# Kernel optimization log

Measured on AMD Instinct MI355X. Metric: run time of the kernel, lower is better.

Reference implementation:

```python
import jax, jax.numpy as jnp
import numpy as np

D_MODEL = 1024
D_HIDDEN = 4096
NUM_EXPERTS = 8
TOP_K = 2


def setup_inputs() -> dict:
    key = jax.random.key(0)
    ks = jax.random.split(key, 7)
    scale_in = 1.0 / np.sqrt(D_MODEL)
    scale_hid = 1.0 / np.sqrt(D_HIDDEN)
    x = jax.random.normal(ks[0], (4, 2048, D_MODEL), dtype=jnp.float32)
    Wr = jax.random.uniform(ks[1], (D_MODEL, NUM_EXPERTS), jnp.float32, -scale_in, scale_in)
    br = jax.random.uniform(ks[2], (NUM_EXPERTS,), jnp.float32, -scale_in, scale_in)
    W1 = jax.random.uniform(ks[3], (NUM_EXPERTS, D_MODEL, D_HIDDEN), jnp.float32, -scale_in, scale_in)
    b1 = jax.random.uniform(ks[4], (NUM_EXPERTS, D_HIDDEN), jnp.float32, -scale_in, scale_in)
    W2 = jax.random.uniform(ks[5], (NUM_EXPERTS, D_HIDDEN, D_MODEL), jnp.float32, -scale_hid, scale_hid)
    b2 = jax.random.uniform(ks[6], (NUM_EXPERTS, D_MODEL), jnp.float32, -scale_hid, scale_hid)
    return {"x": x, "Wr": Wr, "br": br, "W1": W1, "b1": b1, "W2": W2, "b2": b2}


def reference(x, Wr, br, W1, b1, W2, b2):
    B, S, D = x.shape
    E = Wr.shape[1]
    flat = x.reshape(-1, D)                      # [T, D]
    T = flat.shape[0]
    logits = flat @ Wr + br                      # [T, E]
    probs = jax.nn.softmax(logits, axis=-1)
    topk_p, topk_i = jax.lax.top_k(probs, TOP_K)  # [T, K]
    topk_p = topk_p / jnp.sum(topk_p, axis=-1, keepdims=True)
    # combine[t, e] = sum_k topk_p[t, k] * (topk_i[t, k] == e)
    combine = jnp.zeros((T, E), flat.dtype).at[jnp.arange(T)[:, None], topk_i].add(topk_p)
    out = jnp.zeros_like(flat)
    for e in range(E):  # fixed small expert loop; each iter is a dense GEMM pair
        h = jax.nn.relu(flat @ W1[e] + b1[e])    # [T, d_hidden]
        y = h @ W2[e] + b2[e]                    # [T, D]
        out = out + y * combine[:, e:e + 1]
    return out.reshape(B, S, D)
```

## Files before the change

kernel.cpp:

```cpp
#include <hip/hip_runtime.h>
#include <stdint.h>

#define D_MODEL  1024
#define D_HIDDEN 4096
#define NE       8
#define T_TOK    8192
#define BM       128
#define BN       128
#define MAXT     136
#define ROWS_CAP 17408

typedef __attribute__((ext_vector_type(8))) short short8;
typedef __attribute__((ext_vector_type(4))) float f32x4;

__device__ inline uint16_t f2bf(float f) {
  uint32_t u = __float_as_uint(f);
  uint32_t r = (u + 0x7fffu + ((u >> 16) & 1u)) >> 16;
  return (uint16_t)r;
}

#define GLOAD16(gp, lp) __builtin_amdgcn_global_load_lds( \
  (const __attribute__((address_space(1))) uint32_t*)(gp), \
  (__attribute__((address_space(3))) uint32_t*)(lp), 16, 0, 0)

__global__ void transpose_cvt(const float* __restrict__ in, uint16_t* __restrict__ out,
                              int R, int C) {
  __shared__ float tile[32][33];
  size_t eoff = (size_t)blockIdx.z * R * C;
  in += eoff; out += eoff;
  int c0 = blockIdx.x * 32, r0 = blockIdx.y * 32;
  int x = threadIdx.x, y = threadIdx.y;
#pragma unroll
  for (int i = 0; i < 32; i += 8)
    tile[y + i][x] = in[(size_t)(r0 + y + i) * C + c0 + x];
  __syncthreads();
#pragma unroll
  for (int i = 0; i < 32; i += 8)
    out[(size_t)(c0 + y + i) * R + r0 + x] = f2bf(tile[x][y + i]);
}

__global__ void router_kernel(const float* __restrict__ x, const float* __restrict__ Wr,
                              const float* __restrict__ br,
                              int* __restrict__ cnt, int* __restrict__ tok_of,
                              int* __restrict__ k_of, float* __restrict__ tok_w) {
  int t = blockIdx.x * 4 + (threadIdx.x >> 6);
  int l = threadIdx.x & 63;
  const float* xr = x + (size_t)t * D_MODEL;
  float a[8] = {0.f,0.f,0.f,0.f,0.f,0.f,0.f,0.f};
  for (int d = l; d < D_MODEL; d += 64) {
    float xv = xr[d];
    const float4* w4 = (const float4*)(Wr + d * 8);
    float4 wa = w4[0], wb = w4[1];
    a[0] += xv * wa.x; a[1] += xv * wa.y; a[2] += xv * wa.z; a[3] += xv * wa.w;
    a[4] += xv * wb.x; a[5] += xv * wb.y; a[6] += xv * wb.z; a[7] += xv * wb.w;
  }
#pragma unroll
  for (int e = 0; e < 8; ++e) {
    float v = a[e];
#pragma unroll
    for (int off = 32; off > 0; off >>= 1) v += __shfl_xor(v, off);
    a[e] = v + br[e];
  }
  if (l == 0) {
    int i1 = 0; float v1 = a[0];
#pragma unroll
    for (int e = 1; e < 8; ++e) if (a[e] > v1) { v1 = a[e]; i1 = e; }
    int i2 = -1; float v2 = -1e30f;
#pragma unroll
    for (int e = 0; e < 8; ++e) if (e != i1 && a[e] > v2) { v2 = a[e]; i2 = e; }
    float e2 = __expf(v2 - v1);
    float inv = 1.0f / (1.0f + e2);
    int p1 = atomicAdd(cnt + i1, 1);
    tok_of[i1 * T_TOK + p1] = t; k_of[i1 * T_TOK + p1] = 0;
    int p2 = atomicAdd(cnt + i2, 1);
    tok_of[i2 * T_TOK + p2] = t; k_of[i2 * T_TOK + p2] = 1;
    tok_w[t * 2 + 0] = inv; tok_w[t * 2 + 1] = e2 * inv;
  }
}

__global__ void setup_kernel(const int* __restrict__ cnt, int* __restrict__ meta) {
  if (threadIdx.x != 0 || blockIdx.x != 0) return;
  int base = 0, nt = 0;
  meta[1] = 0;
  for (int e = 0; e < NE; ++e) {
    int c = cnt[e];
    int tiles = (c + BM - 1) / BM;
    for (int i = 0; i < tiles; ++i) {
      meta[16 + nt] = e;
      meta[16 + MAXT + nt] = base + i * BM;
      nt++;
    }
    base += tiles * BM;
    meta[2 + e] = base;
  }
  meta[0] = nt;
}

__global__ void gather_kernel(const float* __restrict__ x, const int* __restrict__ cnt,
                              const int* __restrict__ meta, const int* __restrict__ tok_of,
                              const int* __restrict__ k_of, const float* __restrict__ tok_w,
                              uint16_t* __restrict__ xp,
                              int* __restrict__ row2tok, float* __restrict__ row2w) {
  int r = blockIdx.x * 4 + (threadIdx.x >> 6);
  int l = threadIdx.x & 63;
  int total = meta[9];
  if (r >= total) return;
  int e = 0;
#pragma unroll
  for (int i = 1; i < 8; ++i) if (r >= meta[1 + i]) e = i;
  int p = r - meta[1 + e];
  uint16_t* dst = xp + (size_t)r * D_MODEL + l * 16;
  if (p < cnt[e]) {
    int t = tok_of[e * T_TOK + p];
    if (l == 0) {
      row2tok[r] = t;
      row2w[r] = tok_w[t * 2 + k_of[e * T_TOK + p]];
    }
    const float4* src = (const float4*)(x + (size_t)t * D_MODEL + l * 16);
    short8 o0, o1;
    float4 v0 = src[0], v1 = src[1], v2 = src[2], v3 = src[3];
    o0[0] = (short)f2bf(v0.x); o0[1] = (short)f2bf(v0.y);
    o0[2] = (short)f2bf(v0.z); o0[3] = (short)f2bf(v0.w);
    o0[4] = (short)f2bf(v1.x); o0[5] = (short)f2bf(v1.y);
    o0[6] = (short)f2bf(v1.z); o0[7] = (short)f2bf(v1.w);
    o1[0] = (short)f2bf(v2.x); o1[1] = (short)f2bf(v2.y);
    o1[2] = (short)f2bf(v2.z); o1[3] = (short)f2bf(v2.w);
    o1[4] = (short)f2bf(v3.x); o1[5] = (short)f2bf(v3.y);
    o1[6] = (short)f2bf(v3.z); o1[7] = (short)f2bf(v3.w);
    *(short8*)dst = o0;
    *(short8*)(dst + 8) = o1;
  } else {
    if (l == 0) { row2tok[r] = -1; row2w[r] = 0.f; }
    short8 z = {0,0,0,0,0,0,0,0};
    *(short8*)dst = z;
    *(short8*)(dst + 8) = z;
  }
}

template<int KD, int ND, bool FUSED_OUT>
__global__ __launch_bounds__(256, 2) void moe_gemm(
    const uint16_t* __restrict__ A, const uint16_t* __restrict__ Bt,
    const float* __restrict__ bias, uint16_t* __restrict__ Cb,
    float* __restrict__ out, const int* __restrict__ row2tok,
    const float* __restrict__ row2w, const int* __restrict__ meta) {
  int nt = meta[0];
  int mt = blockIdx.y;
  if (mt >= nt) return;
  int e = meta[16 + mt];
  int row0 = meta[16 + MAXT + mt];
  int n0 = blockIdx.x * BN;

  __shared__ __align__(16) uint16_t L[32768];

  int tid = threadIdx.x;
  int l = tid & 63, w = tid >> 6;
  int wrow = w >> 1, wcol = w & 1;
  int arow_r = wrow * 64 + (l & 15);
  int brow_r = wcol * 64 + (l & 15);
  int koff = ((l >> 4) ^ ((l >> 1) & 3)) * 8;

  int r0s = tid >> 2;
  int sseg = (tid & 3) ^ ((r0s >> 1) & 3);
  size_t goA0 = (size_t)r0s * KD + sseg * 8;
  size_t goA1 = (size_t)(r0s + 64) * KD + sseg * 8;

  const uint16_t* Ab = A + (size_t)row0 * KD;
  const uint16_t* Bb = Bt + ((size_t)e * ND + n0) * KD;

  f32x4 acc[4][4];
#pragma unroll
  for (int m = 0; m < 4; ++m)
#pragma unroll
    for (int n = 0; n < 4; ++n) acc[m][n] = (f32x4){0.f, 0.f, 0.f, 0.f};

  auto stage = [&](int buf, int kh, int kt) {
    const uint16_t* ga = Ab + kt * 64 + kh * 32;
    const uint16_t* gb = Bb + kt * 64 + kh * 32;
    uint16_t* lb = L + buf * 16384 + kh * 8192;
    GLOAD16(ga + goA0, lb + tid * 8);
    GLOAD16(ga + goA1, lb + 2048 + tid * 8);
    GLOAD16(gb + goA0, lb + 4096 + tid * 8);
    GLOAD16(gb + goA1, lb + 6144 + tid * 8);
  };

#define PHASE(BUF, KK, DO_STAGE, NKT, VM) do {                                  \
    short8 af[4], bf[4];                                                        \
    const uint16_t* Lb = L + (BUF) * 16384 + (KK) * 8192;                       \
    _Pragma("unroll") for (int m = 0; m < 4; ++m)                               \
      af[m] = *(const short8*)(Lb + (arow_r + m * 16) * 32 + koff);             \
    _Pragma("unroll") for (int n = 0; n < 4; ++n)                               \
      bf[n] = *(const short8*)(Lb + 4096 + (brow_r + n * 16) * 32 + koff);      \
    if (DO_STAGE) stage((BUF) ^ 1, (KK), (NKT));                                \
    asm volatile("s_waitcnt vmcnt(" #VM ")" ::: "memory");                      \
    __builtin_amdgcn_s_barrier();                                               \
    asm volatile("s_waitcnt lgkmcnt(0)" ::: "memory");                          \
    __builtin_amdgcn_sched_barrier(0);                                          \
    __builtin_amdgcn_s_setprio(1);                                              \
    _Pragma("unroll") for (int m = 0; m < 4; ++m)                               \
      _Pragma("unroll") for (int n = 0; n < 4; ++n)                             \
        acc[m][n] = __builtin_amdgcn_mfma_f32_16x16x32_bf16(af[m], bf[n],       \
                                                            acc[m][n], 0, 0, 0);\
    __builtin_amdgcn_s_setprio(0);                                              \
    __builtin_amdgcn_s_barrier();                                               \
  } while (0)

  constexpr int NT = KD / 64;
  stage(0, 0, 0);
  stage(0, 1, 0);
  asm volatile("s_waitcnt vmcnt(4)" ::: "memory");
  __builtin_amdgcn_s_barrier();

  int t = 0;
  for (; t + 2 < NT; t += 2) {
    PHASE(0, 0, true, t + 1, 4);
    PHASE(0, 1, true, t + 1, 4);
    PHASE(1, 0, true, t + 2, 4);
    PHASE(1, 1, true, t + 2, 4);
  }
  PHASE(0, 0, true, NT - 1, 4);
  PHASE(0, 1, true, NT - 1, 4);
  PHASE(1, 0, false, 0, 0);
  PHASE(1, 1, false, 0, 0);
#undef PHASE

  float bv[4];
#pragma unroll
  for (int n = 0; n < 4; ++n)
    bv[n] = bias[e * ND + n0 + wcol * 64 + n * 16 + (l & 15)];

  if (!FUSED_OUT) {
#pragma unroll
    for (int m = 0; m < 4; ++m) {
      int row_b = row0 + wrow * 64 + m * 16 + (l >> 4) * 4;
#pragma unroll
      for (int n = 0; n < 4; ++n) {
        int col = n0 + wcol * 64 + n * 16 + (l & 15);
#pragma unroll
        for (int r = 0; r < 4; ++r)
          Cb[(size_t)(row_b + r) * ND + col] = f2bf(fmaxf(acc[m][n][r] + bv[n], 0.f));
      }
    }
  } else {
#pragma unroll
    for (int m = 0; m < 4; ++m) {
#pragma unroll
      for (int r = 0; r < 4; ++r) {
        int grow = row0 + wrow * 64 + m * 16 + (l >> 4) * 4 + r;
        int tok = row2tok[grow];
        float wgt = row2w[grow];
        if (tok >= 0) {
#pragma unroll
          for (int n = 0; n < 4; ++n) {
            int col = n0 + wcol * 64 + n * 16 + (l & 15);
            atomicAdd(out + (size_t)tok * ND + col, wgt * (acc[m][n][r] + bv[n]));
          }
        }
      }
    }
  }
}

extern "C" void kernel_launch(void* const* d_in, const int* in_sizes, int n_in,
                              void* d_out, int out_size, void* d_ws, size_t ws_size,
                              hipStream_t stream) {
  const float* x  = (const float*)d_in[0];
  const float* Wr = (const float*)d_in[1];
  const float* br = (const float*)d_in[2];
  const float* W1 = (const float*)d_in[3];
  const float* b1 = (const float*)d_in[4];
  const float* W2 = (const float*)d_in[5];
  const float* b2 = (const float*)d_in[6];
  float* out = (float*)d_out;

  char* ws = (char*)d_ws;
  size_t off = 0;
  auto alloc = [&](size_t bytes) -> void* {
    void* p = ws + off;
    off += (bytes + 255) & ~(size_t)255;
    return p;
  };
  uint16_t* W1T    = (uint16_t*)alloc((size_t)NE * D_MODEL * D_HIDDEN * 2);
  uint16_t* W2T    = (uint16_t*)alloc((size_t)NE * D_MODEL * D_HIDDEN * 2);
  uint16_t* xp     = (uint16_t*)alloc((size_t)ROWS_CAP * D_MODEL * 2);
  uint16_t* hp     = (uint16_t*)alloc((size_t)ROWS_CAP * D_HIDDEN * 2);
  int*      cnt    = (int*)alloc(NE * 4);
  int*      tok_of = (int*)alloc((size_t)NE * T_TOK * 4);
  int*      k_of   = (int*)alloc((size_t)NE * T_TOK * 4);
  float*    tok_w  = (float*)alloc(T_TOK * 2 * 4);
  int*      row2tok= (int*)alloc(ROWS_CAP * 4);
  float*    row2w  = (float*)alloc(ROWS_CAP * 4);
  int*      meta   = (int*)alloc((16 + 2 * MAXT) * 4);

  if (ws_size < off) return;

  hipMemsetAsync(cnt, 0, NE * 4, stream);
  hipMemsetAsync(out, 0, (size_t)out_size * 4, stream);
  transpose_cvt<<<dim3(D_HIDDEN / 32, D_MODEL / 32, NE), dim3(32, 8), 0, stream>>>(
      W1, W1T, D_MODEL, D_HIDDEN);
  transpose_cvt<<<dim3(D_MODEL / 32, D_HIDDEN / 32, NE), dim3(32, 8), 0, stream>>>(
      W2, W2T, D_HIDDEN, D_MODEL);
  router_kernel<<<T_TOK / 4, 256, 0, stream>>>(x, Wr, br, cnt, tok_of, k_of, tok_w);
  setup_kernel<<<1, 64, 0, stream>>>(cnt, meta);
  gather_kernel<<<ROWS_CAP / 4, 256, 0, stream>>>(x, cnt, meta, tok_of, k_of, tok_w,
                                                  xp, row2tok, row2w);
  moe_gemm<D_MODEL, D_HIDDEN, false><<<dim3(D_HIDDEN / BN, MAXT), 256, 0, stream>>>(
      xp, W1T, b1, hp, nullptr, nullptr, nullptr, meta);
  moe_gemm<D_HIDDEN, D_MODEL, true><<<dim3(D_MODEL / BN, MAXT), 256, 0, stream>>>(
      hp, W2T, b2, nullptr, out, row2tok, row2w, meta);
}
```

Measured before the change: 746.4 us.

## Enlarge MoE GEMM tiles to 256x256 with 8 waves, triple-buffer, split-K, and swizzle

```diff
diff --git a/kernel.cpp b/kernel.cpp
--- a/kernel.cpp
+++ b/kernel.cpp
@@ -5,10 +5,10 @@
 #define D_HIDDEN 4096
 #define NE       8
 #define T_TOK    8192
-#define BM       128
-#define BN       128
-#define MAXT     136
-#define ROWS_CAP 17408
+#define BM       256
+#define BN       256
+#define MAXT     72
+#define ROWS_CAP 18432
 
 typedef __attribute__((ext_vector_type(8))) short short8;
 typedef __attribute__((ext_vector_type(4))) float f32x4;
@@ -25,18 +25,28 @@
 
 __global__ void transpose_cvt(const float* __restrict__ in, uint16_t* __restrict__ out,
                               int R, int C) {
-  __shared__ float tile[32][33];
+  __shared__ float tile[64][65];
   size_t eoff = (size_t)blockIdx.z * R * C;
-  in += eoff; out += eoff;
-  int c0 = blockIdx.x * 32, r0 = blockIdx.y * 32;
-  int x = threadIdx.x, y = threadIdx.y;
-#pragma unroll
-  for (int i = 0; i < 32; i += 8)
-    tile[y + i][x] = in[(size_t)(r0 + y + i) * C + c0 + x];
+  int c0 = blockIdx.x * 64, r0 = blockIdx.y * 64;
+  int t = threadIdx.x;
+  int lr = t >> 4, lc4 = (t & 15) * 4;
+#pragma unroll
+  for (int i = 0; i < 4; ++i) {
+    int rr = i * 16 + lr;
+    float4 v = *(const float4*)(in + eoff + (size_t)(r0 + rr) * C + c0 + lc4);
+    tile[rr][lc4] = v.x; tile[rr][lc4 + 1] = v.y;
+    tile[rr][lc4 + 2] = v.z; tile[rr][lc4 + 3] = v.w;
+  }
   __syncthreads();
-#pragma unroll
-  for (int i = 0; i < 32; i += 8)
-    out[(size_t)(c0 + y + i) * R + r0 + x] = f2bf(tile[x][y + i]);
+  int oc = t >> 3, orr = (t & 7) * 8;
+#pragma unroll
+  for (int i = 0; i < 2; ++i) {
+    int cc = i * 32 + oc;
+    short8 o;
+#pragma unroll
+    for (int j = 0; j < 8; ++j) o[j] = (short)f2bf(tile[orr + j][cc]);
+    *(short8*)(out + eoff + (size_t)(c0 + cc) * R + r0 + orr) = o;
+  }
 }
 
 __global__ void router_kernel(const float* __restrict__ x, const float* __restrict__ Wr,
@@ -137,122 +147,142 @@
   }
 }
 
-template<int KD, int ND, bool FUSED_OUT>
-__global__ __launch_bounds__(256, 2) void moe_gemm(
+template<int KD, int ND, int KSPLIT, bool FUSED_OUT>
+__global__ __launch_bounds__(512, 2) void moe_gemm(
     const uint16_t* __restrict__ A, const uint16_t* __restrict__ Bt,
     const float* __restrict__ bias, uint16_t* __restrict__ Cb,
     float* __restrict__ out, const int* __restrict__ row2tok,
     const float* __restrict__ row2w, const int* __restrict__ meta) {
+  constexpr int NTX = ND / BN;
+  constexpr int KS  = KD / KSPLIT;
+  constexpr int NT  = KS / 32;
+  constexpr int NWG = NTX * MAXT;
+
+  int bid = blockIdx.y * NTX + blockIdx.x;
+  int bid2 = (bid & 7) * (NWG >> 3) + (bid >> 3);
+  int mt = bid2 / NTX;
   int nt = meta[0];
-  int mt = blockIdx.y;
   if (mt >= nt) return;
+  int n0 = (bid2 % NTX) * BN;
   int e = meta[16 + mt];
   int row0 = meta[16 + MAXT + mt];
-  int n0 = blockIdx.x * BN;
-
-  __shared__ __align__(16) uint16_t L[32768];
+  int ks = blockIdx.z;
+
+  __shared__ __align__(16) uint16_t L[49152];
 
   int tid = threadIdx.x;
   int l = tid & 63, w = tid >> 6;
-  int wrow = w >> 1, wcol = w & 1;
-  int arow_r = wrow * 64 + (l & 15);
-  int brow_r = wcol * 64 + (l & 15);
-  int koff = ((l >> 4) ^ ((l >> 1) & 3)) * 8;
-
-  int r0s = tid >> 2;
-  int sseg = (tid & 3) ^ ((r0s >> 1) & 3);
-  size_t goA0 = (size_t)r0s * KD + sseg * 8;
-  size_t goA1 = (size_t)(r0s + 64) * KD + sseg * 8;
-
-  const uint16_t* Ab = A + (size_t)row0 * KD;
-  const uint16_t* Bb = Bt + ((size_t)e * ND + n0) * KD;
-
-  f32x4 acc[4][4];
-#pragma unroll
-  for (int m = 0; m < 4; ++m)
+  int wrow = w >> 2, wcol = w & 3;
+  int swz = ((l >> 4) ^ (l & 3)) * 8;
+  int arow_base = (wrow * 128 + (l & 15)) * 32 + swz;
+  int brow_base = 8192 + (wcol * 64 + (l & 15)) * 32 + swz;
+
+  int sr = tid >> 2;
+  size_t s_src = (size_t)sr * KD + ((tid & 3) ^ (sr & 3)) * 8;
+  int s_dst = tid * 8;
+
+  const uint16_t* Ab = A + (size_t)row0 * KD + ks * KS;
+  const uint16_t* Bb = Bt + ((size_t)e * ND + n0) * KD + ks * KS;
+
+  f32x4 acc[8][4];
+#pragma unroll
+  for (int m = 0; m < 8; ++m)
 #pragma unroll
     for (int n = 0; n < 4; ++n) acc[m][n] = (f32x4){0.f, 0.f, 0.f, 0.f};
 
-  auto stage = [&](int buf, int kh, int kt) {
-    const uint16_t* ga = Ab + kt * 64 + kh * 32;
-    const uint16_t* gb = Bb + kt * 64 + kh * 32;
-    uint16_t* lb = L + buf * 16384 + kh * 8192;
-    GLOAD16(ga + goA0, lb + tid * 8);
-    GLOAD16(ga + goA1, lb + 2048 + tid * 8);
-    GLOAD16(gb + goA0, lb + 4096 + tid * 8);
-    GLOAD16(gb + goA1, lb + 6144 + tid * 8);
+  auto stageA = [&](int sb, int kt) {
+    const uint16_t* ga = Ab + kt * 32;
+    uint16_t* ld = L + sb * 16384;
+    GLOAD16(ga + s_src, ld + s_dst);
+    GLOAD16(ga + s_src + (size_t)128 * KD, ld + s_dst + 4096);
   };
-
-#define PHASE(BUF, KK, DO_STAGE, NKT, VM) do {                                  \
-    short8 af[4], bf[4];                                                        \
-    const uint16_t* Lb = L + (BUF) * 16384 + (KK) * 8192;                       \
-    _Pragma("unroll") for (int m = 0; m < 4; ++m)                               \
-      af[m] = *(const short8*)(Lb + (arow_r + m * 16) * 32 + koff);             \
-    _Pragma("unroll") for (int n = 0; n < 4; ++n)                               \
-      bf[n] = *(const short8*)(Lb + 4096 + (brow_r + n * 16) * 32 + koff);      \
-    if (DO_STAGE) stage((BUF) ^ 1, (KK), (NKT));                                \
-    asm volatile("s_waitcnt vmcnt(" #VM ")" ::: "memory");                      \
-    __builtin_amdgcn_s_barrier();                                               \
-    asm volatile("s_waitcnt lgkmcnt(0)" ::: "memory");                          \
-    __builtin_amdgcn_sched_barrier(0);                                          \
-    __builtin_amdgcn_s_setprio(1);                                              \
-    _Pragma("unroll") for (int m = 0; m < 4; ++m)                               \
-      _Pragma("unroll") for (int n = 0; n < 4; ++n)                             \
-        acc[m][n] = __builtin_amdgcn_mfma_f32_16x16x32_bf16(af[m], bf[n],       \
-                                                            acc[m][n], 0, 0, 0);\
-    __builtin_amdgcn_s_setprio(0);                                              \
-    __builtin_amdgcn_s_barrier();                                               \
+  auto stageB = [&](int sb, int kt) {
+    const uint16_t* gb = Bb + kt * 32;
+    uint16_t* ld = L + sb * 16384 + 8192;
+    GLOAD16(gb + s_src, ld + s_dst);
+    GLOAD16(gb + s_src + (size_t)128 * KD, ld + s_dst + 4096);
+  };
+
+#define TILE(B0, DO_ST, SB, KT2, VM) do {                                        \
+    const uint16_t* Lb = L + (B0) * 16384;                                       \
+    short8 af[4], bfr[4];                                                        \
+    _Pragma("unroll") for (int n = 0; n < 4; ++n)                                \
+      bfr[n] = *(const short8*)(Lb + brow_base + n * 512);                       \
+    _Pragma("unroll") for (int m = 0; m < 4; ++m)                                \
+      af[m] = *(const short8*)(Lb + arow_base + m * 512);                        \
+    if (DO_ST) stageA(SB, KT2);                                                  \
+    __builtin_amdgcn_s_barrier();                                                \
+    asm volatile("s_waitcnt lgkmcnt(0)" ::: "memory");                           \
+    __builtin_amdgcn_sched_barrier(0);                                           \
+    __builtin_amdgcn_s_setprio(1);                                               \
+    _Pragma("unroll") for (int m = 0; m < 4; ++m)                                \
+      _Pragma("unroll") for (int n = 0; n < 4; ++n)                              \
+        acc[m][n] = __builtin_amdgcn_mfma_f32_16x16x32_bf16(af[m], bfr[n],       \
+                                                            acc[m][n], 0, 0, 0); \
+    __builtin_amdgcn_s_setprio(0);                                               \
+    __builtin_amdgcn_s_barrier();                                                \
+    _Pragma("unroll") for (int m = 0; m < 4; ++m)                                \
+      af[m] = *(const short8*)(Lb + arow_base + 2048 + m * 512);                 \
+    if (DO_ST) stageB(SB, KT2);                                                  \
+    asm volatile("s_waitcnt vmcnt(" VM ")" ::: "memory");                        \
+    __builtin_amdgcn_s_barrier();                                                \
+    asm volatile("s_waitcnt lgkmcnt(0)" ::: "memory");                           \
+    __builtin_amdgcn_sched_barrier(0);                                           \
+    __builtin_amdgcn_s_setprio(1);                                               \
+    _Pragma("unroll") for (int m = 0; m < 4; ++m)                                \
+      _Pragma("unroll") for (int n = 0; n < 4; ++n)                              \
+        acc[4 + m][n] = __builtin_amdgcn_mfma_f32_16x16x32_bf16(af[m], bfr[n],   \
+                                                         acc[4 + m][n], 0, 0, 0);\
+    __builtin_amdgcn_s_setprio(0);                                               \
+    __builtin_amdgcn_s_barrier();                                                \
   } while (0)
 
-  constexpr int NT = KD / 64;
-  stage(0, 0, 0);
-  stage(0, 1, 0);
+  stageA(0, 0); stageB(0, 0);
+  stageA(1, 1); stageB(1, 1);
   asm volatile("s_waitcnt vmcnt(4)" ::: "memory");
   __builtin_amdgcn_s_barrier();
 
-  int t = 0;
-  for (; t + 2 < NT; t += 2) {
-    PHASE(0, 0, true, t + 1, 4);
-    PHASE(0, 1, true, t + 1, 4);
-    PHASE(1, 0, true, t + 2, 4);
-    PHASE(1, 1, true, t + 2, 4);
-  }
-  PHASE(0, 0, true, NT - 1, 4);
-  PHASE(0, 1, true, NT - 1, 4);
-  PHASE(1, 0, false, 0, 0);
-  PHASE(1, 1, false, 0, 0);
-#undef PHASE
-
-  float bv[4];
-#pragma unroll
-  for (int n = 0; n < 4; ++n)
-    bv[n] = bias[e * ND + n0 + wcol * 64 + n * 16 + (l & 15)];
+  int b0 = 0;
+  for (int t = 0; t + 2 < NT; ++t) {
+    int sb = b0 + 2; if (sb >= 3) sb -= 3;
+    TILE(b0, 1, sb, t + 2, "4");
+    b0 = (b0 == 2) ? 0 : b0 + 1;
+  }
+  TILE(b0, 0, 0, 0, "0");
+  b0 = (b0 == 2) ? 0 : b0 + 1;
+  TILE(b0, 0, 0, 0, "0");
+#undef TILE
 
   if (!FUSED_OUT) {
 #pragma unroll
-    for (int m = 0; m < 4; ++m) {
-      int row_b = row0 + wrow * 64 + m * 16 + (l >> 4) * 4;
+    for (int mf = 0; mf < 8; ++mf) {
+      int rbase = row0 + wrow * 128 + mf * 16 + (l >> 4) * 4;
 #pragma unroll
       for (int n = 0; n < 4; ++n) {
         int col = n0 + wcol * 64 + n * 16 + (l & 15);
+        float bv = bias[e * ND + col];
 #pragma unroll
         for (int r = 0; r < 4; ++r)
-          Cb[(size_t)(row_b + r) * ND + col] = f2bf(fmaxf(acc[m][n][r] + bv[n], 0.f));
+          Cb[(size_t)(rbase + r) * ND + col] = f2bf(fmaxf(acc[mf][n][r] + bv, 0.f));
       }
     }
   } else {
-#pragma unroll
-    for (int m = 0; m < 4; ++m) {
+    float bv[4];
+#pragma unroll
+    for (int n = 0; n < 4; ++n)
+      bv[n] = (ks == 0) ? bias[e * ND + n0 + wcol * 64 + n * 16 + (l & 15)] : 0.f;
+#pragma unroll
+    for (int mf = 0; mf < 8; ++mf) {
 #pragma unroll
       for (int r = 0; r < 4; ++r) {
-        int grow = row0 + wrow * 64 + m * 16 + (l >> 4) * 4 + r;
+        int grow = row0 + wrow * 128 + mf * 16 + (l >> 4) * 4 + r;
         int tok = row2tok[grow];
         float wgt = row2w[grow];
         if (tok >= 0) {
 #pragma unroll
           for (int n = 0; n < 4; ++n) {
             int col = n0 + wcol * 64 + n * 16 + (l & 15);
-            atomicAdd(out + (size_t)tok * ND + col, wgt * (acc[m][n][r] + bv[n]));
+            atomicAdd(out + (size_t)tok * ND + col, wgt * (acc[mf][n][r] + bv[n]));
           }
         }
       }
@@ -295,16 +325,16 @@
 
   hipMemsetAsync(cnt, 0, NE * 4, stream);
   hipMemsetAsync(out, 0, (size_t)out_size * 4, stream);
-  transpose_cvt<<<dim3(D_HIDDEN / 32, D_MODEL / 32, NE), dim3(32, 8), 0, stream>>>(
+  transpose_cvt<<<dim3(D_HIDDEN / 64, D_MODEL / 64, NE), 256, 0, stream>>>(
       W1, W1T, D_MODEL, D_HIDDEN);
-  transpose_cvt<<<dim3(D_MODEL / 32, D_HIDDEN / 32, NE), dim3(32, 8), 0, stream>>>(
+  transpose_cvt<<<dim3(D_MODEL / 64, D_HIDDEN / 64, NE), 256, 0, stream>>>(
       W2, W2T, D_HIDDEN, D_MODEL);
   router_kernel<<<T_TOK / 4, 256, 0, stream>>>(x, Wr, br, cnt, tok_of, k_of, tok_w);
   setup_kernel<<<1, 64, 0, stream>>>(cnt, meta);
   gather_kernel<<<ROWS_CAP / 4, 256, 0, stream>>>(x, cnt, meta, tok_of, k_of, tok_w,
                                                   xp, row2tok, row2w);
-  moe_gemm<D_MODEL, D_HIDDEN, false><<<dim3(D_HIDDEN / BN, MAXT), 256, 0, stream>>>(
+  moe_gemm<D_MODEL, D_HIDDEN, 1, false><<<dim3(D_HIDDEN / BN, MAXT, 1), 512, 0, stream>>>(
       xp, W1T, b1, hp, nullptr, nullptr, nullptr, meta);
-  moe_gemm<D_HIDDEN, D_MODEL, true><<<dim3(D_MODEL / BN, MAXT), 256, 0, stream>>>(
+  moe_gemm<D_HIDDEN, D_MODEL, 2, true><<<dim3(D_MODEL / BN, MAXT, 2), 512, 0, stream>>>(
       hp, W2T, b2, nullptr, out, row2tok, row2w, meta);
 }
```

Result: slower. 771.8 us (+3.4%).
